# Kernel tuning notes

Measured on AMD Instinct MI355X. Metric: run time of the kernel, lower is better.

Reference implementation:

```python
import jax, jax.numpy as jnp
import numpy as np

B, C_IN, C_OUT, H, W, K = 64, 64, 128, 64, 64, 3


def setup_inputs() -> dict:
    key = jax.random.key(0)
    k1, k2, k3 = jax.random.split(key, 3)
    x = jax.random.normal(k1, (B, C_IN, H, W), dtype=jnp.float32)
    weight = jax.random.normal(k2, (C_OUT, C_IN, K, K), dtype=jnp.float32)
    bias = jax.random.normal(k3, (C_OUT, 1, 1), dtype=jnp.float32)
    return {"x": x, "weight": weight, "bias": bias}


def reference(x, weight, bias):
    # Valid (no pad), stride-1, NCHW direct conv + broadcast bias, matching
    # the naive nested-loop conv2d_multi_in_out + bias of MyConv2D.
    out = jax.lax.conv_general_dilated(
        x, weight,
        window_strides=(1, 1),
        padding="VALID",
        dimension_numbers=("NCHW", "OIHW", "NCHW"),
    )
    return out + bias  # bias (C_out,1,1) broadcasts over (B, C_out, H_out, W_out)
```

## Files before the change

kernel.cpp:

```cpp
#include <hip/hip_runtime.h>

#define CI 64
#define CO 128
#define HH 64
#define WW 64
#define OH 62
#define OW 62
#define XTW 66
#define RB (XTW * 64)
#define ROWS_OUT 4
#define ROWS_IN 6
#define NBLK_X 16

typedef __attribute__((ext_vector_type(8))) short short8x;
typedef __attribute__((ext_vector_type(16))) float f32x16;

__device__ __attribute__((aligned(16))) ushort g_wt[9 * CO * CI];

__device__ __forceinline__ ushort bf16rne(float f) {
    unsigned u = __builtin_bit_cast(unsigned, f);
    u += 0x7fffu + ((u >> 16) & 1u);
    return (ushort)(u >> 16);
}

__global__ __launch_bounds__(256)
void wprep(const float* __restrict__ w) {
    const int idx = blockIdx.x * 256 + threadIdx.x;
    const int kk = idx >> 13;
    const int rem = idx & 8191;
    const int co = rem >> 6, ci = rem & 63;
    g_wt[idx] = bf16rne(w[(co * 64 + ci) * 9 + kk]);
}

__global__ __launch_bounds__(256, 2)
void conv_fused(const float* __restrict__ x, const float* __restrict__ bias,
                float* __restrict__ out) {
    __shared__ ushort Xl[ROWS_IN * RB];
    __shared__ float  sB[CO];

    const int tid = threadIdx.x;
    const int wv = tid >> 6, L = tid & 63, l31 = L & 31, q = L >> 5;
    const int h = wv >> 1;
    const int rw = wv & 1;
    const int b = blockIdx.y, oh0 = blockIdx.x * ROWS_OUT;

    if (tid < CO) sB[tid] = bias[tid];

    const ushort* wbase = g_wt + (h * 64 + l31) * 64 + q * 8;
    short8x wbuf[2][8];
    #pragma unroll
    for (int m = 0; m < 2; ++m)
        #pragma unroll
        for (int ss = 0; ss < 4; ++ss)
            wbuf[0][m * 4 + ss] = *(const short8x*)(wbase + m * 2048 + ss * 16);

    if (tid < 96) {
        const int r6 = tid >> 4, c = tid & 15;
        const int px = 64 + (c >> 3), slot = c & 7;
        const uint4 z{0, 0, 0, 0};
        *reinterpret_cast<uint4*>(&Xl[(r6 * XTW + px) * 64 + slot * 8]) = z;
    }

    const int w = L;
    const size_t cibase = (size_t)(b * 64 + wv * 16) * (HH * WW);
    #pragma unroll
    for (int r6 = 0; r6 < 4; ++r6) {
        const int ir = oh0 + r6;
        const float* src = x + cibase + (size_t)ir * WW + w;
        union { ushort u[8]; uint4 v; } p0, p1;
        #pragma unroll
        for (int k = 0; k < 8; ++k)
            p0.u[k] = bf16rne(src[(size_t)k * (HH * WW)]);
        #pragma unroll
        for (int k = 0; k < 8; ++k)
            p1.u[k] = bf16rne(src[(size_t)(8 + k) * (HH * WW)]);
        const int pl = r6 * XTW + w, key = pl & 7;
        ushort* dst = &Xl[pl * 64];
        *reinterpret_cast<uint4*>(dst + (((2 * wv)     ^ key) * 8)) = p0.v;
        *reinterpret_cast<uint4*>(dst + (((2 * wv + 1) ^ key) * 8)) = p1.v;
    }

    f32x16 acc[2][2][2];
    #pragma unroll
    for (int r2 = 0; r2 < 2; ++r2)
        #pragma unroll
        for (int i = 0; i < 2; ++i)
            #pragma unroll
            for (int jj = 0; jj < 2; ++jj)
                #pragma unroll
                for (int r = 0; r < 16; ++r) acc[r2][i][jj][r] = 0.f;

    __syncthreads();

    float v45[2][16];
    #pragma unroll
    for (int r2 = 0; r2 < 2; ++r2) {
        int ir = oh0 + 4 + r2;
        if (ir > 63) ir = 63;
        const float* src = x + cibase + (size_t)ir * WW + w;
        #pragma unroll
        for (int k = 0; k < 16; ++k)
            v45[r2][k] = src[(size_t)k * (HH * WW)];
    }

    #pragma unroll
    for (int kk = 0; kk < 3; ++kk) {
        const short8x* wf = wbuf[kk & 1];
        {
            const ushort* nb = wbase + (kk + 1) * (CO * CI);
            #pragma unroll
            for (int m = 0; m < 2; ++m)
                #pragma unroll
                for (int ss = 0; ss < 4; ++ss)
                    wbuf[(kk + 1) & 1][m * 4 + ss] = *(const short8x*)(nb + m * 2048 + ss * 16);
        }
        const int kc = kk;
        const int pBa = rw * XTW + kc + l31;
        const int pBb = (rw + 2) * XTW + kc + l31;
        const ushort* bPa = Xl + pBa * 64;
        const ushort* bPb = Xl + pBb * 64;
        const int f0a = pBa & 7, f0b = pBb & 7;
        #pragma unroll
        for (int ss = 0; ss < 4; ++ss) {
            const int oba = (((ss * 2 + q) ^ f0a) * 8);
            const int obb = (((ss * 2 + q) ^ f0b) * 8);
            short8x a0 = *(const short8x*)(bPa + oba);
            short8x a1 = *(const short8x*)(bPa + 32 * 64 + oba);
            short8x c0 = *(const short8x*)(bPb + obb);
            short8x c1 = *(const short8x*)(bPb + 32 * 64 + obb);
            acc[0][0][0] = __builtin_amdgcn_mfma_f32_32x32x16_bf16(wf[ss],     a0, acc[0][0][0], 0, 0, 0);
            acc[0][0][1] = __builtin_amdgcn_mfma_f32_32x32x16_bf16(wf[ss],     a1, acc[0][0][1], 0, 0, 0);
            acc[0][1][0] = __builtin_amdgcn_mfma_f32_32x32x16_bf16(wf[4 + ss], a0, acc[0][1][0], 0, 0, 0);
            acc[0][1][1] = __builtin_amdgcn_mfma_f32_32x32x16_bf16(wf[4 + ss], a1, acc[0][1][1], 0, 0, 0);
            acc[1][0][0] = __builtin_amdgcn_mfma_f32_32x32x16_bf16(wf[ss],     c0, acc[1][0][0], 0, 0, 0);
            acc[1][0][1] = __builtin_amdgcn_mfma_f32_32x32x16_bf16(wf[ss],     c1, acc[1][0][1], 0, 0, 0);
            acc[1][1][0] = __builtin_amdgcn_mfma_f32_32x32x16_bf16(wf[4 + ss], c0, acc[1][1][0], 0, 0, 0);
            acc[1][1][1] = __builtin_amdgcn_mfma_f32_32x32x16_bf16(wf[4 + ss], c1, acc[1][1][1], 0, 0, 0);
        }
    }

    #pragma unroll
    for (int r2 = 0; r2 < 2; ++r2) {
        union { ushort u[8]; uint4 v; } p0, p1;
        #pragma unroll
        for (int k = 0; k < 8; ++k) p0.u[k] = bf16rne(v45[r2][k]);
        #pragma unroll
        for (int k = 0; k < 8; ++k) p1.u[k] = bf16rne(v45[r2][8 + k]);
        const int pl = (4 + r2) * XTW + w, key = pl & 7;
        ushort* dst = &Xl[pl * 64];
        *reinterpret_cast<uint4*>(dst + (((2 * wv)     ^ key) * 8)) = p0.v;
        *reinterpret_cast<uint4*>(dst + (((2 * wv + 1) ^ key) * 8)) = p1.v;
    }

    __syncthreads();

    #pragma unroll
    for (int kk = 3; kk < 9; ++kk) {
        const short8x* wf = wbuf[kk & 1];
        if (kk < 8) {
            const ushort* nb = wbase + (kk + 1) * (CO * CI);
            #pragma unroll
            for (int m = 0; m < 2; ++m)
                #pragma unroll
                for (int ss = 0; ss < 4; ++ss)
                    wbuf[(kk + 1) & 1][m * 4 + ss] = *(const short8x*)(nb + m * 2048 + ss * 16);
        }
        const int kr = kk / 3, kc = kk - kr * 3;
        const int pBa = (rw + kr) * XTW + kc + l31;
        const int pBb = (rw + 2 + kr) * XTW + kc + l31;
        const ushort* bPa = Xl + pBa * 64;
        const ushort* bPb = Xl + pBb * 64;
        const int f0a = pBa & 7, f0b = pBb & 7;
        #pragma unroll
        for (int ss = 0; ss < 4; ++ss) {
            const int oba = (((ss * 2 + q) ^ f0a) * 8);
            const int obb = (((ss * 2 + q) ^ f0b) * 8);
            short8x a0 = *(const short8x*)(bPa + oba);
            short8x a1 = *(const short8x*)(bPa + 32 * 64 + oba);
            short8x c0 = *(const short8x*)(bPb + obb);
            short8x c1 = *(const short8x*)(bPb + 32 * 64 + obb);
            acc[0][0][0] = __builtin_amdgcn_mfma_f32_32x32x16_bf16(wf[ss],     a0, acc[0][0][0], 0, 0, 0);
            acc[0][0][1] = __builtin_amdgcn_mfma_f32_32x32x16_bf16(wf[ss],     a1, acc[0][0][1], 0, 0, 0);
            acc[0][1][0] = __builtin_amdgcn_mfma_f32_32x32x16_bf16(wf[4 + ss], a0, acc[0][1][0], 0, 0, 0);
            acc[0][1][1] = __builtin_amdgcn_mfma_f32_32x32x16_bf16(wf[4 + ss], a1, acc[0][1][1], 0, 0, 0);
            acc[1][0][0] = __builtin_amdgcn_mfma_f32_32x32x16_bf16(wf[ss],     c0, acc[1][0][0], 0, 0, 0);
            acc[1][0][1] = __builtin_amdgcn_mfma_f32_32x32x16_bf16(wf[ss],     c1, acc[1][0][1], 0, 0, 0);
            acc[1][1][0] = __builtin_amdgcn_mfma_f32_32x32x16_bf16(wf[4 + ss], c0, acc[1][1][0], 0, 0, 0);
            acc[1][1][1] = __builtin_amdgcn_mfma_f32_32x32x16_bf16(wf[4 + ss], c1, acc[1][1][1], 0, 0, 0);
        }
    }

    #pragma unroll
    for (int r2 = 0; r2 < 2; ++r2) {
        const int oh = oh0 + rw + 2 * r2;
        if (oh < OH) {
            #pragma unroll
            for (int mt = 0; mt < 2; ++mt)
                #pragma unroll
                for (int nt = 0; nt < 2; ++nt) {
                    const int col = nt * 32 + l31;
                    if (col < OW) {
                        #pragma unroll
                        for (int reg = 0; reg < 16; ++reg) {
                            const int co = h * 64 + mt * 32 + 4 * q + (reg & 3) + 8 * (reg >> 2);
                            out[(((size_t)b * CO + co) * OH + oh) * OW + col] = acc[r2][mt][nt][reg] + sB[co];
                        }
                    }
                }
        }
    }
}

extern "C" void kernel_launch(void* const* d_in, const int* in_sizes, int n_in,
                              void* d_out, int out_size, void* d_ws, size_t ws_size,
                              hipStream_t stream) {
    const float* x    = (const float*)d_in[0];
    const float* wgt  = (const float*)d_in[1];
    const float* bias = (const float*)d_in[2];
    float* out = (float*)d_out;

    wprep<<<dim3(288), 256, 0, stream>>>(wgt);
    conv_fused<<<dim3(NBLK_X, 64), 256, 0, stream>>>(x, bias, out);
}
```

Measured before the change: 214.9 us.

## Process eight output rows per block using a ring-buffered LDS tile

Each block now computes eight output rows in two passes of four. Input rows sit in an eight-slot ring buffer in LDS, so the two overlapping halo rows are loaded once and reused across both passes. Weights are reloaded from global memory for the second pass. This halves the block count and cuts redundant input loads and conversions, but it needs more LDS per block and the first pass's stores now run in the middle of the kernel.

Result: slower. 306.4 us (+42.6%).

```diff
diff --git a/kernel.cpp b/kernel.cpp
--- a/kernel.cpp
+++ b/kernel.cpp
@@ -8,9 +8,9 @@
 #define OW 62
 #define XTW 66
 #define RB (XTW * 64)
-#define ROWS_OUT 4
-#define ROWS_IN 6
-#define NBLK_X 16
+#define ROWS_OUT 8
+#define NSLOT 8
+#define NBLK_X 8
 
 typedef __attribute__((ext_vector_type(8))) short short8x;
 typedef __attribute__((ext_vector_type(16))) float f32x16;
@@ -35,7 +35,7 @@
 __global__ __launch_bounds__(256, 2)
 void conv_fused(const float* __restrict__ x, const float* __restrict__ bias,
                 float* __restrict__ out) {
-    __shared__ ushort Xl[ROWS_IN * RB];
+    __shared__ ushort Xl[NSLOT * RB];
     __shared__ float  sB[CO];
 
     const int tid = threadIdx.x;
@@ -54,18 +54,19 @@
         for (int ss = 0; ss < 4; ++ss)
             wbuf[0][m * 4 + ss] = *(const short8x*)(wbase + m * 2048 + ss * 16);
 
-    if (tid < 96) {
-        const int r6 = tid >> 4, c = tid & 15;
+    if (tid < 128) {
+        const int s8 = tid >> 4, c = tid & 15;
         const int px = 64 + (c >> 3), slot = c & 7;
         const uint4 z{0, 0, 0, 0};
-        *reinterpret_cast<uint4*>(&Xl[(r6 * XTW + px) * 64 + slot * 8]) = z;
+        *reinterpret_cast<uint4*>(&Xl[(s8 * XTW + px) * 64 + slot * 8]) = z;
     }
 
     const int w = L;
     const size_t cibase = (size_t)(b * 64 + wv * 16) * (HH * WW);
     #pragma unroll
-    for (int r6 = 0; r6 < 4; ++r6) {
-        const int ir = oh0 + r6;
+    for (int r8 = 0; r8 < 8; ++r8) {
+        int ir = oh0 + r8;
+        if (ir > 63) ir = 63;
         const float* src = x + cibase + (size_t)ir * WW + w;
         union { ushort u[8]; uint4 v; } p0, p1;
         #pragma unroll
@@ -74,7 +75,7 @@
         #pragma unroll
         for (int k = 0; k < 8; ++k)
             p1.u[k] = bf16rne(src[(size_t)(8 + k) * (HH * WW)]);
-        const int pl = r6 * XTW + w, key = pl & 7;
+        const int pl = r8 * XTW + w, key = pl & 7;
         ushort* dst = &Xl[pl * 64];
         *reinterpret_cast<uint4*>(dst + (((2 * wv)     ^ key) * 8)) = p0.v;
         *reinterpret_cast<uint4*>(dst + (((2 * wv + 1) ^ key) * 8)) = p1.v;
@@ -92,21 +93,21 @@
 
     __syncthreads();
 
-    float v45[2][16];
-    #pragma unroll
-    for (int r2 = 0; r2 < 2; ++r2) {
-        int ir = oh0 + 4 + r2;
+    float v89[2][16];
+    #pragma unroll
+    for (int r2 = 0; r2 < 2; ++r2) {
+        int ir = oh0 + 8 + r2;
         if (ir > 63) ir = 63;
         const float* src = x + cibase + (size_t)ir * WW + w;
         #pragma unroll
         for (int k = 0; k < 16; ++k)
-            v45[r2][k] = src[(size_t)k * (HH * WW)];
-    }
-
-    #pragma unroll
-    for (int kk = 0; kk < 3; ++kk) {
+            v89[r2][k] = src[(size_t)k * (HH * WW)];
+    }
+
+    #pragma unroll
+    for (int kk = 0; kk < 9; ++kk) {
         const short8x* wf = wbuf[kk & 1];
-        {
+        if (kk < 8) {
             const ushort* nb = wbase + (kk + 1) * (CO * CI);
             #pragma unroll
             for (int m = 0; m < 2; ++m)
@@ -114,9 +115,9 @@
                 for (int ss = 0; ss < 4; ++ss)
                     wbuf[(kk + 1) & 1][m * 4 + ss] = *(const short8x*)(nb + m * 2048 + ss * 16);
         }
-        const int kc = kk;
-        const int pBa = rw * XTW + kc + l31;
-        const int pBb = (rw + 2) * XTW + kc + l31;
+        const int kr = kk / 3, kc = kk - kr * 3;
+        const int pBa = (rw + kr) * XTW + kc + l31;
+        const int pBb = (rw + 2 + kr) * XTW + kc + l31;
         const ushort* bPa = Xl + pBa * 64;
         const ushort* bPb = Xl + pBb * 64;
         const int f0a = pBa & 7, f0b = pBb & 7;
@@ -139,14 +140,16 @@
         }
     }
 
+    __syncthreads();
+
     #pragma unroll
     for (int r2 = 0; r2 < 2; ++r2) {
         union { ushort u[8]; uint4 v; } p0, p1;
         #pragma unroll
-        for (int k = 0; k < 8; ++k) p0.u[k] = bf16rne(v45[r2][k]);
-        #pragma unroll
-        for (int k = 0; k < 8; ++k) p1.u[k] = bf16rne(v45[r2][8 + k]);
-        const int pl = (4 + r2) * XTW + w, key = pl & 7;
+        for (int k = 0; k < 8; ++k) p0.u[k] = bf16rne(v89[r2][k]);
+        #pragma unroll
+        for (int k = 0; k < 8; ++k) p1.u[k] = bf16rne(v89[r2][8 + k]);
+        const int pl = r2 * XTW + w, key = pl & 7;
         ushort* dst = &Xl[pl * 64];
         *reinterpret_cast<uint4*>(dst + (((2 * wv)     ^ key) * 8)) = p0.v;
         *reinterpret_cast<uint4*>(dst + (((2 * wv + 1) ^ key) * 8)) = p1.v;
@@ -155,7 +158,40 @@
     __syncthreads();
 
     #pragma unroll
-    for (int kk = 3; kk < 9; ++kk) {
+    for (int m = 0; m < 2; ++m)
+        #pragma unroll
+        for (int ss = 0; ss < 4; ++ss)
+            wbuf[0][m * 4 + ss] = *(const short8x*)(wbase + m * 2048 + ss * 16);
+
+    #pragma unroll
+    for (int r2 = 0; r2 < 2; ++r2) {
+        const int oh = oh0 + rw + 2 * r2;
+        #pragma unroll
+        for (int mt = 0; mt < 2; ++mt)
+            #pragma unroll
+            for (int nt = 0; nt < 2; ++nt) {
+                const int col = nt * 32 + l31;
+                if (col < OW) {
+                    #pragma unroll
+                    for (int reg = 0; reg < 16; ++reg) {
+                        const int co = h * 64 + mt * 32 + 4 * q + (reg & 3) + 8 * (reg >> 2);
+                        out[(((size_t)b * CO + co) * OH + oh) * OW + col] = acc[r2][mt][nt][reg] + sB[co];
+                    }
+                }
+            }
+    }
+
+    #pragma unroll
+    for (int r2 = 0; r2 < 2; ++r2)
+        #pragma unroll
+        for (int i = 0; i < 2; ++i)
+            #pragma unroll
+            for (int jj = 0; jj < 2; ++jj)
+                #pragma unroll
+                for (int r = 0; r < 16; ++r) acc[r2][i][jj][r] = 0.f;
+
+    #pragma unroll
+    for (int kk = 0; kk < 9; ++kk) {
         const short8x* wf = wbuf[kk & 1];
         if (kk < 8) {
             const ushort* nb = wbase + (kk + 1) * (CO * CI);
@@ -166,8 +202,10 @@
                     wbuf[(kk + 1) & 1][m * 4 + ss] = *(const short8x*)(nb + m * 2048 + ss * 16);
         }
         const int kr = kk / 3, kc = kk - kr * 3;
-        const int pBa = (rw + kr) * XTW + kc + l31;
-        const int pBb = (rw + 2 + kr) * XTW + kc + l31;
+        const int sa = (4 + rw + kr) & 7;
+        const int sb2 = (6 + rw + kr) & 7;
+        const int pBa = sa * XTW + kc + l31;
+        const int pBb = sb2 * XTW + kc + l31;
         const ushort* bPa = Xl + pBa * 64;
         const ushort* bPb = Xl + pBb * 64;
         const int f0a = pBa & 7, f0b = pBb & 7;
@@ -192,7 +230,7 @@
 
     #pragma unroll
     for (int r2 = 0; r2 < 2; ++r2) {
-        const int oh = oh0 + rw + 2 * r2;
+        const int oh = oh0 + 4 + rw + 2 * r2;
         if (oh < OH) {
             #pragma unroll
             for (int mt = 0; mt < 2; ++mt)
```
